# Performance work log

Hardware: AMD Instinct MI355X
Metric: run time of the kernel (lower is better)

## Reference

```python
import jax, jax.numpy as jnp
import numpy as np

B, L, C, K = 4, 32768, 64, 7
NORM_FACTOR = 1.0
EPS = 1e-5


def setup_inputs() -> dict:
    key = jax.random.key(0)
    ks = jax.random.split(key, 7)
    return {
        "x": jax.random.normal(ks[0], (B, L, C), jnp.float32),
        "weights": jax.random.normal(ks[1], (C, C, K), jnp.float32) * 0.05,  # ~lecun scale
        "w_conv": jax.random.normal(ks[2], (C, C), jnp.float32) * 0.125,
        "scale1": jax.random.uniform(ks[3], (C,), jnp.float32, 0.5, 1.5),
        "bias1": jax.random.normal(ks[4], (C,), jnp.float32) * 0.1,
        "scale2": jax.random.uniform(ks[5], (C,), jnp.float32, 0.5, 1.5),
        "bias2": jax.random.normal(ks[6], (C,), jnp.float32) * 0.1,
    }


def _batchnorm(x, scale, bias):
    # train-mode BatchNorm: stats over (batch, length), feature axis last
    mean = jnp.mean(x, axis=(0, 1), keepdims=True)
    var = jnp.var(x, axis=(0, 1), keepdims=True)
    return (x - mean) * jax.lax.rsqrt(var + EPS) * scale + bias


def reference(x, weights, w_conv, scale1, bias1, scale2, bias2):
    b, l, c = x.shape
    k = weights.shape[-1]
    x_ = x
    # unfold: windows of 2K at stride 2 -> (B, C*2K, T) -> (B, C, T, 2K)
    p = jax.lax.conv_general_dilated_patches(
        jnp.transpose(x, (0, 2, 1)), filter_shape=(2 * k,),
        window_strides=(2,), padding=((0, 0),))
    t = p.shape[-1]
    xp = jnp.transpose(jnp.reshape(p, (b, c, 2 * k, t)), (0, 1, 3, 2))
    # dynamic gate weights: (B, 2T, C) x (Cout, Cin, K) -> (B, Cout, 2T, K)
    w = jnp.einsum('blc,dck->bdlk', x_[:, -(2 * t):, :], weights)
    even_seq = w[:, :, ::2, :]   # (B, C, T, K)
    odd_seq = w[:, :, 1::2, :]   # (B, C, T, K)
    w = jnp.reshape(jnp.stack([even_seq, odd_seq], axis=-1), (b, c, t, 2 * k))
    w = jnp.tanh(w / NORM_FACTOR)
    y = jnp.sum(xp * w, axis=3)            # (B, C, T)
    y = jnp.transpose(y, (0, 2, 1))        # (B, T, C)
    y = x_[:, ::2, :][:, -t:, :] + y       # skip and inner_skip
    y = _batchnorm(y, scale1, bias1)
    y_ = y
    z = y @ w_conv                          # 1x1 conv, no bias
    z = _batchnorm(z, scale2, bias2)
    z = jax.nn.gelu(z)                      # approximate=True, matches flax default
    return y_ + z
```

## Files before the change

kernel.cpp:

```cpp
#include <hip/hip_runtime.h>
#include <hip/hip_bf16.h>

#define B_ 4
#define L_ 32768
#define C_ 64
#define K_ 7
#define T_ 16378
#define M_ (B_*T_)
#define TJ 16
#define IT 4
#define NJB 256
#define NBLKA (B_*NJB)
#define NBZ 512
#define NBE 1024

#define OF_WB   0
#define OF_WB2  14336
#define OF_Y    16384
#define OF_PS1  (OF_Y + M_*32)
#define OF_PQ1  (OF_PS1 + 64*NBLKA)
#define OF_PS2  (OF_PQ1 + 64*NBLKA)
#define OF_PQ2  (OF_PS2 + 64*NBZ)
#define OF_C1   (OF_PQ2 + 64*NBZ)
#define OF_C2   (OF_C1 + 128)

typedef __attribute__((ext_vector_type(8))) short short8;
typedef __attribute__((ext_vector_type(4))) float f32x4;

__device__ __forceinline__ unsigned cvt_pk_bf16(float a, float b) {
    unsigned r;
    asm("v_cvt_pk_bf16_f32 %0, %1, %2" : "=v"(r) : "v"(a), "v"(b));
    return r;
}

__device__ __forceinline__ float fast_tanh(float x) {
    float e = __builtin_amdgcn_exp2f(x * 2.885390082f);
    return __builtin_fmaf(-2.f, __builtin_amdgcn_rcpf(1.f + e), 1.f);
}

__device__ __forceinline__ float gelu_tanh(float v) {
    float u = 0.7978845608028654f * (v + 0.044715f * v * v * v);
    return 0.5f * v * (1.f + fast_tanh(u));
}

__device__ __forceinline__ float bfu(ushort h) {
    union { unsigned u; float f; } v; v.u = ((unsigned)h) << 16; return v.f;
}

__global__ void kPb(const float* __restrict__ w, ushort* __restrict__ Wb) {
    int i = blockIdx.x * 256 + threadIdx.x;
    if (i < 28672) {
        int j = i & 7;
        int l = (i >> 3) & 63;
        int q = i >> 9;
        int nt = q % 28, kt = q / 28;
        int k = kt * 32 + 8 * (l >> 4) + j;
        int n = nt * 16 + (l & 15);
        int d = n / 7, kk = n - 7 * d;
        Wb[i] = (ushort)(cvt_pk_bf16(w[(d * 64 + k) * 7 + kk], 0.f) & 0xffffu);
    }
}

__global__ __launch_bounds__(256, 4) void kA(const float* __restrict__ x,
                                             const ushort* __restrict__ Wb,
                                             ushort* __restrict__ y,
                                             float* __restrict__ ps,
                                             float* __restrict__ pq) {
    __shared__ ushort xp[22 * 128];
    __shared__ ushort gsT[448 * 34];
    __shared__ float  red[2][4][64];

    const int tid = threadIdx.x;
    const int w = tid >> 6, l = tid & 63;
    const int b = blockIdx.y;
    const float* xb = x + (long)b * L_ * 64;

    short8 wreg[7][2];
    #pragma unroll
    for (int i = 0; i < 7; ++i) {
        wreg[i][0] = *(const short8*)&Wb[((w + 4 * i) * 64 + l) * 8];
        wreg[i][1] = *(const short8*)&Wb[((28 + w + 4 * i) * 64 + l) * 8];
    }

    float S = 0.f, Q = 0.f;

    for (int it = 0; it < IT; ++it) {
        const int jt = blockIdx.x * IT + it;
        const int j0 = jt * TJ;
        const int xrow0 = 2 * j0;
        if (it) __syncthreads();

        #pragma unroll
        for (int st = 0; st < 3; ++st) {
            int p = tid + st * 256;
            if (p < 704) {
                int rp = p >> 5, c0 = (p & 31) * 2;
                int r0 = min(xrow0 + 2 * rp, L_ - 1);
                int r1 = min(xrow0 + 2 * rp + 1, L_ - 1);
                float2 va = *(const float2*)(xb + (long)r0 * 64 + c0);
                float2 vb = *(const float2*)(xb + (long)r1 * 64 + c0);
                uint2 wv;
                wv.x = cvt_pk_bf16(va.x, vb.x);
                wv.y = cvt_pk_bf16(va.y, vb.y);
                *(uint2*)((char*)xp + rp * 256 + c0 * 4) = wv;
            }
        }

        short8 afr[2][2];
        #pragma unroll
        for (int mt = 0; mt < 2; ++mt)
            #pragma unroll
            for (int kt = 0; kt < 2; ++kt) {
                int row = min(xrow0 + 12 + mt * 16 + (l & 15), L_ - 1);
                const float* pr = xb + (long)row * 64 + kt * 32 + (l >> 4) * 8;
                float4 v0 = *(const float4*)pr;
                float4 v1 = *(const float4*)(pr + 4);
                uint4 u;
                u.x = cvt_pk_bf16(v0.x, v0.y);
                u.y = cvt_pk_bf16(v0.z, v0.w);
                u.z = cvt_pk_bf16(v1.x, v1.y);
                u.w = cvt_pk_bf16(v1.z, v1.w);
                afr[mt][kt] = *(short8*)&u;
            }

        {
            const int col = l & 15;
            const int r0 = 4 * (l >> 4);
            #pragma unroll
            for (int i = 0; i < 7; ++i) {
                const int nt = w + 4 * i;
                f32x4 acc0 = {0.f, 0.f, 0.f, 0.f};
                f32x4 acc1 = {0.f, 0.f, 0.f, 0.f};
                acc0 = __builtin_amdgcn_mfma_f32_16x16x32_bf16(afr[0][0], wreg[i][0], acc0, 0, 0, 0);
                acc0 = __builtin_amdgcn_mfma_f32_16x16x32_bf16(afr[0][1], wreg[i][1], acc0, 0, 0, 0);
                acc1 = __builtin_amdgcn_mfma_f32_16x16x32_bf16(afr[1][0], wreg[i][0], acc1, 0, 0, 0);
                acc1 = __builtin_amdgcn_mfma_f32_16x16x32_bf16(afr[1][1], wreg[i][1], acc1, 0, 0, 0);
                const int n = nt * 16 + col;
                char* base = (char*)gsT + n * 68;
                *(unsigned*)(base + r0 * 2)            = cvt_pk_bf16(fast_tanh(acc0[0]), fast_tanh(acc0[1]));
                *(unsigned*)(base + r0 * 2 + 4)        = cvt_pk_bf16(fast_tanh(acc0[2]), fast_tanh(acc0[3]));
                *(unsigned*)(base + (r0 + 16) * 2)     = cvt_pk_bf16(fast_tanh(acc1[0]), fast_tanh(acc1[1]));
                *(unsigned*)(base + (r0 + 16) * 2 + 4) = cvt_pk_bf16(fast_tanh(acc1[2]), fast_tanh(acc1[3]));
            }
        }
        __syncthreads();

        #pragma unroll
        for (int ii = 0; ii < 4; ++ii) {
            const int jj = w + 4 * ii;
            const int j = j0 + jj;
            float acc = bfu(*(const ushort*)((const char*)xp + (6 + jj) * 256 + l * 4));
            const char* xbp = (const char*)xp + jj * 256 + l * 4;
            const char* gbp = (const char*)gsT + l * 476 + jj * 4;
            #pragma unroll
            for (int kk = 0; kk < K_; ++kk) {
                unsigned xpr = *(const unsigned*)(xbp + kk * 256);
                unsigned gp  = *(const unsigned*)(gbp + kk * 68);
                asm("v_dot2_f32_bf16 %0, %1, %2, %0" : "+v"(acc) : "v"(xpr), "v"(gp));
            }
            float other = __shfl_xor(acc, 1);
            if (j < T_) {
                if ((l & 1) == 0) {
                    *(unsigned*)((char*)y + ((long)(b * T_ + j)) * 128 + l * 2) = cvt_pk_bf16(acc, other);
                }
                S += acc;
                Q += acc * acc;
            }
        }
    }

    red[0][w][l] = S;
    red[1][w][l] = Q;
    __syncthreads();
    if (tid < 64) {
        float S4 = red[0][0][tid] + red[0][1][tid] + red[0][2][tid] + red[0][3][tid];
        float Q4 = red[1][0][tid] + red[1][1][tid] + red[1][2][tid] + red[1][3][tid];
        int blk = b * NJB + blockIdx.x;
        ps[tid * NBLKA + blk] = S4;
        pq[tid * NBLKA + blk] = Q4;
    }
}

__global__ void kB(const float* __restrict__ ps, const float* __restrict__ pq,
                   float* __restrict__ A, float* __restrict__ BB,
                   const float* __restrict__ scale, const float* __restrict__ bias,
                   int nblk, float invN) {
    const int c = blockIdx.x;
    const float* bs = ps + (long)c * nblk;
    const float* bq = pq + (long)c * nblk;
    float S = 0.f, Q = 0.f;
    for (int i = threadIdx.x; i < nblk; i += 256) {
        S += bs[i];
        Q += bq[i];
    }
    for (int o = 32; o > 0; o >>= 1) {
        S += __shfl_down(S, o);
        Q += __shfl_down(Q, o);
    }
    __shared__ float rs[4], rq[4];
    if ((threadIdx.x & 63) == 0) { rs[threadIdx.x >> 6] = S; rq[threadIdx.x >> 6] = Q; }
    __syncthreads();
    if (threadIdx.x == 0) {
        S = rs[0] + rs[1] + rs[2] + rs[3];
        Q = rq[0] + rq[1] + rq[2] + rq[3];
        float m = S * invN;
        float var = Q * invN - m * m;
        float rstd = rsqrtf(var + 1e-5f);
        float a = rstd * scale[c];
        A[c] = a;
        BB[c] = bias[c] - m * a;
    }
}

__global__ void kW(const float* __restrict__ wconv, const float* __restrict__ A1,
                   ushort* __restrict__ Wb2) {
    int i = blockIdx.x * 256 + threadIdx.x;
    if (i < 4096) {
        int j = i & 7, lane = (i >> 3) & 63, q2 = i >> 9;
        int kt = q2 >> 2, nt = q2 & 3;
        int c = kt * 32 + 8 * (lane >> 4) + j;
        int e = nt * 16 + (lane & 15);
        Wb2[i] = (ushort)(cvt_pk_bf16(A1[c] * wconv[c * 64 + e], 0.f) & 0xffffu);
    }
}

__global__ __launch_bounds__(256) void kZ(const ushort* __restrict__ y,
                                          const ushort* __restrict__ Wb2,
                                          float* __restrict__ ps2,
                                          float* __restrict__ pq2) {
    __shared__ float red[2][4][64];
    const int tid = threadIdx.x, w = tid >> 6, l = tid & 63;
    short8 bfr[4][2];
    #pragma unroll
    for (int nt = 0; nt < 4; ++nt)
        #pragma unroll
        for (int kt = 0; kt < 2; ++kt)
            bfr[nt][kt] = *(const short8*)&Wb2[((kt * 4 + nt) * 64 + l) * 8];

    float ss[4] = {0.f, 0.f, 0.f, 0.f}, qq[4] = {0.f, 0.f, 0.f, 0.f};
    #pragma unroll
    for (int g2 = 0; g2 < 2; ++g2) {
        long rowg = (long)blockIdx.x * 128 + g2 * 64 + w * 16 + (l & 15);
        short8 a0 = {0, 0, 0, 0, 0, 0, 0, 0};
        short8 a1 = {0, 0, 0, 0, 0, 0, 0, 0};
        if (rowg < M_) {
            const char* yr = (const char*)y + rowg * 128 + (l >> 4) * 16;
            a0 = *(const short8*)yr;
            a1 = *(const short8*)(yr + 64);
        }
        #pragma unroll
        for (int nt = 0; nt < 4; ++nt) {
            f32x4 acc = {0.f, 0.f, 0.f, 0.f};
            acc = __builtin_amdgcn_mfma_f32_16x16x32_bf16(a0, bfr[nt][0], acc, 0, 0, 0);
            acc = __builtin_amdgcn_mfma_f32_16x16x32_bf16(a1, bfr[nt][1], acc, 0, 0, 0);
            #pragma unroll
            for (int i = 0; i < 4; ++i) { ss[nt] += acc[i]; qq[nt] += acc[i] * acc[i]; }
        }
    }
    #pragma unroll
    for (int nt = 0; nt < 4; ++nt) {
        float s2 = ss[nt] + __shfl_xor(ss[nt], 16); s2 += __shfl_xor(s2, 32);
        float q2 = qq[nt] + __shfl_xor(qq[nt], 16); q2 += __shfl_xor(q2, 32);
        if (l < 16) { red[0][w][nt * 16 + l] = s2; red[1][w][nt * 16 + l] = q2; }
    }
    __syncthreads();
    if (tid < 64) {
        float S = red[0][0][tid] + red[0][1][tid] + red[0][2][tid] + red[0][3][tid];
        float Q = red[1][0][tid] + red[1][1][tid] + red[1][2][tid] + red[1][3][tid];
        ps2[tid * NBZ + blockIdx.x] = S;
        pq2[tid * NBZ + blockIdx.x] = Q;
    }
}

__global__ __launch_bounds__(256) void kE(const ushort* __restrict__ y,
                                          const ushort* __restrict__ Wb2,
                                          const float* __restrict__ A1,
                                          const float* __restrict__ B1,
                                          const float* __restrict__ A2,
                                          const float* __restrict__ B2,
                                          float* __restrict__ out) {
    const int tid = threadIdx.x, w = tid >> 6, l = tid & 63;
    short8 bfr[4][2];
    #pragma unroll
    for (int nt = 0; nt < 4; ++nt)
        #pragma unroll
        for (int kt = 0; kt < 2; ++kt)
            bfr[nt][kt] = *(const short8*)&Wb2[((kt * 4 + nt) * 64 + l) * 8];

    const long row0 = (long)blockIdx.x * 64;
    long rowg = row0 + w * 16 + (l & 15);
    short8 a0 = {0, 0, 0, 0, 0, 0, 0, 0};
    short8 a1 = {0, 0, 0, 0, 0, 0, 0, 0};
    if (rowg < M_) {
        const char* yr = (const char*)y + rowg * 128 + (l >> 4) * 16;
        a0 = *(const short8*)yr;
        a1 = *(const short8*)(yr + 64);
    }
    #pragma unroll
    for (int nt = 0; nt < 4; ++nt) {
        f32x4 acc = {0.f, 0.f, 0.f, 0.f};
        acc = __builtin_amdgcn_mfma_f32_16x16x32_bf16(a0, bfr[nt][0], acc, 0, 0, 0);
        acc = __builtin_amdgcn_mfma_f32_16x16x32_bf16(a1, bfr[nt][1], acc, 0, 0, 0);
        const int e = nt * 16 + (l & 15);
        const float a1c = A1[e], b1c = B1[e], a2c = A2[e], b2c = B2[e];
        #pragma unroll
        for (int i = 0; i < 4; ++i) {
            long gr = row0 + w * 16 + 4 * (l >> 4) + i;
            if (gr < M_) {
                float yv = bfu(*(const ushort*)((const char*)y + gr * 128 + e * 2));
                float zb = a2c * acc[i] + b2c;
                out[gr * 64 + e] = fmaf(a1c, yv, b1c) + gelu_tanh(zb);
            }
        }
    }
}

extern "C" void kernel_launch(void* const* d_in, const int* in_sizes, int n_in,
                              void* d_out, int out_size, void* d_ws, size_t ws_size,
                              hipStream_t stream) {
    const float* x       = (const float*)d_in[0];
    const float* weights = (const float*)d_in[1];
    const float* w_conv  = (const float*)d_in[2];
    const float* scale1  = (const float*)d_in[3];
    const float* bias1   = (const float*)d_in[4];
    const float* scale2  = (const float*)d_in[5];
    const float* bias2   = (const float*)d_in[6];
    float* out = (float*)d_out;
    float* ws  = (float*)d_ws;

    ushort* Wb  = (ushort*)(ws + OF_WB);
    ushort* Wb2 = (ushort*)(ws + OF_WB2);
    ushort* yb  = (ushort*)(ws + OF_Y);
    float* ps1 = ws + OF_PS1;
    float* pq1 = ws + OF_PQ1;
    float* ps2 = ws + OF_PS2;
    float* pq2 = ws + OF_PQ2;
    float* A1  = ws + OF_C1;
    float* BB1 = ws + OF_C1 + 64;
    float* A2  = ws + OF_C2;
    float* BB2 = ws + OF_C2 + 64;

    const float invN = 1.f / (float)M_;

    kPb<<<112, 256, 0, stream>>>(weights, Wb);
    kA<<<dim3(NJB, B_), 256, 0, stream>>>(x, Wb, yb, ps1, pq1);
    kB<<<64, 256, 0, stream>>>(ps1, pq1, A1, BB1, scale1, bias1, NBLKA, invN);
    kW<<<16, 256, 0, stream>>>(w_conv, A1, Wb2);
    kZ<<<NBZ, 256, 0, stream>>>(yb, Wb2, ps2, pq2);
    kB<<<64, 256, 0, stream>>>(ps2, pq2, A2, BB2, scale2, bias2, NBZ, invN);
    kE<<<NBE, 256, 0, stream>>>(yb, Wb2, A1, BB1, A2, BB2, out);
}
```

Measured before the change: 60.79 us.

## Vectorize gate LDS stores, pair output rows in kA, stage kE epilogue via LDS

In kA, the gate tile rows are padded to 72 bytes and written as 8-byte stores. The weighted-sum stage now computes two adjacent output rows per iteration, reusing the x-patch words it has loaded and reading gate pairs with 8-byte loads. In kE, the MFMA results go into a shared tile first, then each thread reads the bf16 y values and writes the outputs as coalesced float4 vectors, with the BN coefficients cached in LDS. The aim is to cut scalar, scattered global stores and redundant LDS loads, at the cost of more shared memory and an extra barrier in kE.

New measurement: 59.21 us. 1.03x faster.

```diff
diff --git a/kernel.cpp b/kernel.cpp
--- a/kernel.cpp
+++ b/kernel.cpp
@@ -46,6 +46,9 @@
 __device__ __forceinline__ float bfu(ushort h) {
     union { unsigned u; float f; } v; v.u = ((unsigned)h) << 16; return v.f;
 }
+__device__ __forceinline__ float bflo(unsigned p) {
+    union { unsigned u; float f; } v; v.u = p << 16; return v.f;
+}
 
 __global__ void kPb(const float* __restrict__ w, ushort* __restrict__ Wb) {
     int i = blockIdx.x * 256 + threadIdx.x;
@@ -67,7 +70,7 @@
                                              float* __restrict__ ps,
                                              float* __restrict__ pq) {
     __shared__ ushort xp[22 * 128];
-    __shared__ ushort gsT[448 * 34];
+    __shared__ ushort gsT[448 * 36];
     __shared__ float  red[2][4][64];
 
     const int tid = threadIdx.x;
@@ -136,35 +139,44 @@
                 acc1 = __builtin_amdgcn_mfma_f32_16x16x32_bf16(afr[1][0], wreg[i][0], acc1, 0, 0, 0);
                 acc1 = __builtin_amdgcn_mfma_f32_16x16x32_bf16(afr[1][1], wreg[i][1], acc1, 0, 0, 0);
                 const int n = nt * 16 + col;
-                char* base = (char*)gsT + n * 68;
-                *(unsigned*)(base + r0 * 2)            = cvt_pk_bf16(fast_tanh(acc0[0]), fast_tanh(acc0[1]));
-                *(unsigned*)(base + r0 * 2 + 4)        = cvt_pk_bf16(fast_tanh(acc0[2]), fast_tanh(acc0[3]));
-                *(unsigned*)(base + (r0 + 16) * 2)     = cvt_pk_bf16(fast_tanh(acc1[0]), fast_tanh(acc1[1]));
-                *(unsigned*)(base + (r0 + 16) * 2 + 4) = cvt_pk_bf16(fast_tanh(acc1[2]), fast_tanh(acc1[3]));
+                char* base = (char*)gsT + n * 72;
+                uint2 lo, hi;
+                lo.x = cvt_pk_bf16(fast_tanh(acc0[0]), fast_tanh(acc0[1]));
+                lo.y = cvt_pk_bf16(fast_tanh(acc0[2]), fast_tanh(acc0[3]));
+                hi.x = cvt_pk_bf16(fast_tanh(acc1[0]), fast_tanh(acc1[1]));
+                hi.y = cvt_pk_bf16(fast_tanh(acc1[2]), fast_tanh(acc1[3]));
+                *(uint2*)(base + r0 * 2)      = lo;
+                *(uint2*)(base + 32 + r0 * 2) = hi;
             }
         }
         __syncthreads();
 
         #pragma unroll
-        for (int ii = 0; ii < 4; ++ii) {
-            const int jj = w + 4 * ii;
-            const int j = j0 + jj;
-            float acc = bfu(*(const ushort*)((const char*)xp + (6 + jj) * 256 + l * 4));
-            const char* xbp = (const char*)xp + jj * 256 + l * 4;
-            const char* gbp = (const char*)gsT + l * 476 + jj * 4;
+        for (int jp = 0; jp < 2; ++jp) {
+            const int jj0 = 2 * w + 8 * jp;
+            unsigned xv[8];
+            #pragma unroll
+            for (int k2 = 0; k2 < 8; ++k2)
+                xv[k2] = *(const unsigned*)((const char*)xp + (jj0 + k2) * 256 + l * 4);
+            float acc0 = bflo(xv[6]);
+            float acc1 = bflo(xv[7]);
+            const char* gbp = (const char*)gsT + l * 504 + jj0 * 4;
             #pragma unroll
             for (int kk = 0; kk < K_; ++kk) {
-                unsigned xpr = *(const unsigned*)(xbp + kk * 256);
-                unsigned gp  = *(const unsigned*)(gbp + kk * 68);
-                asm("v_dot2_f32_bf16 %0, %1, %2, %0" : "+v"(acc) : "v"(xpr), "v"(gp));
-            }
-            float other = __shfl_xor(acc, 1);
+                uint2 gp = *(const uint2*)(gbp + kk * 72);
+                asm("v_dot2_f32_bf16 %0, %1, %2, %0" : "+v"(acc0) : "v"(xv[kk]),     "v"(gp.x));
+                asm("v_dot2_f32_bf16 %0, %1, %2, %0" : "+v"(acc1) : "v"(xv[kk + 1]), "v"(gp.y));
+            }
+            float o0 = __shfl_xor(acc0, 1);
+            float o1 = __shfl_xor(acc1, 1);
+            const int j = j0 + jj0;
             if (j < T_) {
                 if ((l & 1) == 0) {
-                    *(unsigned*)((char*)y + ((long)(b * T_ + j)) * 128 + l * 2) = cvt_pk_bf16(acc, other);
+                    *(unsigned*)((char*)y + (long)(b * T_ + j) * 128 + l * 2)     = cvt_pk_bf16(acc0, o0);
+                    *(unsigned*)((char*)y + (long)(b * T_ + j + 1) * 128 + l * 2) = cvt_pk_bf16(acc1, o1);
                 }
-                S += acc;
-                Q += acc * acc;
+                S += acc0 + acc1;
+                Q += acc0 * acc0 + acc1 * acc1;
             }
         }
     }
@@ -279,7 +291,15 @@
                                           const float* __restrict__ A2,
                                           const float* __restrict__ B2,
                                           float* __restrict__ out) {
+    __shared__ float zs[64][68];
+    __shared__ float cf[4][64];
     const int tid = threadIdx.x, w = tid >> 6, l = tid & 63;
+
+    if (tid < 64)       cf[0][tid] = A1[tid];
+    else if (tid < 128) cf[1][tid - 64] = B1[tid - 64];
+    else if (tid < 192) cf[2][tid - 128] = A2[tid - 128];
+    else                cf[3][tid - 192] = B2[tid - 192];
+
     short8 bfr[4][2];
     #pragma unroll
     for (int nt = 0; nt < 4; ++nt)
@@ -302,15 +322,28 @@
         acc = __builtin_amdgcn_mfma_f32_16x16x32_bf16(a0, bfr[nt][0], acc, 0, 0, 0);
         acc = __builtin_amdgcn_mfma_f32_16x16x32_bf16(a1, bfr[nt][1], acc, 0, 0, 0);
         const int e = nt * 16 + (l & 15);
-        const float a1c = A1[e], b1c = B1[e], a2c = A2[e], b2c = B2[e];
-        #pragma unroll
-        for (int i = 0; i < 4; ++i) {
-            long gr = row0 + w * 16 + 4 * (l >> 4) + i;
-            if (gr < M_) {
-                float yv = bfu(*(const ushort*)((const char*)y + gr * 128 + e * 2));
-                float zb = a2c * acc[i] + b2c;
-                out[gr * 64 + e] = fmaf(a1c, yv, b1c) + gelu_tanh(zb);
-            }
+        #pragma unroll
+        for (int i = 0; i < 4; ++i)
+            zs[w * 16 + 4 * (l >> 4) + i][e] = acc[i];
+    }
+    __syncthreads();
+
+    #pragma unroll
+    for (int i = 0; i < 4; ++i) {
+        int rloc = i * 16 + (tid >> 4);
+        long gr = row0 + rloc;
+        int ch0 = (tid & 15) * 4;
+        if (gr < M_) {
+            uint2 yp = *(const uint2*)((const char*)y + gr * 128 + ch0 * 2);
+            float4 z4 = *(const float4*)&zs[rloc][ch0];
+            float yv0 = bflo(yp.x), yv1 = bfu((ushort)(yp.x >> 16));
+            float yv2 = bflo(yp.y), yv3 = bfu((ushort)(yp.y >> 16));
+            float4 o;
+            o.x = fmaf(cf[0][ch0 + 0], yv0, cf[1][ch0 + 0]) + gelu_tanh(fmaf(cf[2][ch0 + 0], z4.x, cf[3][ch0 + 0]));
+            o.y = fmaf(cf[0][ch0 + 1], yv1, cf[1][ch0 + 1]) + gelu_tanh(fmaf(cf[2][ch0 + 1], z4.y, cf[3][ch0 + 1]));
+            o.z = fmaf(cf[0][ch0 + 2], yv2, cf[1][ch0 + 2]) + gelu_tanh(fmaf(cf[2][ch0 + 2], z4.z, cf[3][ch0 + 2]));
+            o.w = fmaf(cf[0][ch0 + 3], yv3, cf[1][ch0 + 3]) + gelu_tanh(fmaf(cf[2][ch0 + 3], z4.w, cf[3][ch0 + 3]));
+            *(float4*)&out[gr * 64 + ch0] = o;
         }
     }
 }
```
